# Kernel tuning notes

Hardware: AMD Instinct MI355X
Metric: run time of the kernel (lower is better)

Reference implementation:

```python
import jax
import jax.numpy as jnp
from jax import lax
import numpy as np

VOCAB = 50000
EMBED = 300
HIDDEN = 256
BATCH = 64
SEQ = 256
FORGET_BIAS = 1.0


def setup_inputs() -> dict:
    key = jax.random.key(0)
    k = jax.random.split(key, 6)
    x_in = jax.random.randint(k[0], (BATCH, SEQ), 0, VOCAB, dtype=jnp.int64)
    embedding = jax.random.normal(k[1], (VOCAB, EMBED), dtype=jnp.float32)
    W0 = jax.random.normal(k[2], (EMBED + HIDDEN, 4 * HIDDEN), dtype=jnp.float32) * 0.05
    b0 = jnp.zeros((4 * HIDDEN,), dtype=jnp.float32)
    W1 = jax.random.normal(k[3], (HIDDEN + HIDDEN, 4 * HIDDEN), dtype=jnp.float32) * 0.05
    b1 = jnp.zeros((4 * HIDDEN,), dtype=jnp.float32)
    return {"x_in": x_in, "embedding": embedding, "W0": W0, "b0": b0, "W1": W1, "b1": b1}


def _lstm_layer(xs, W, b):
    # xs: [B, T, D] -> hidden sequence [B, T, H] (BasicLSTMCell, gate order i,j,f,o)
    B = xs.shape[0]
    H = W.shape[1] // 4

    def step(carry, x_t):
        c, h = carry
        gates = jnp.dot(jnp.concatenate([x_t, h], axis=-1), W) + b  # [B, 4H]
        i, j, f, o = jnp.split(gates, 4, axis=-1)
        new_c = c * jax.nn.sigmoid(f + FORGET_BIAS) + jax.nn.sigmoid(i) * jnp.tanh(j)
        new_h = jnp.tanh(new_c) * jax.nn.sigmoid(o)
        return (new_c, new_h), new_h

    init = (jnp.zeros((B, H), xs.dtype), jnp.zeros((B, H), xs.dtype))
    _, hs = lax.scan(step, init, jnp.swapaxes(xs, 0, 1))  # hs: [T, B, H]
    return jnp.swapaxes(hs, 0, 1)


def reference(x_in, embedding, W0, b0, W1, b1):
    word_vecs = embedding[x_in]                 # [B, T, E] frozen embedding lookup
    h1 = _lstm_layer(word_vecs, W0, b0)         # layer 1
    h2 = _lstm_layer(h1, W1, b1)                # layer 2
    return h2[:, -1, :]                          # output at last timestep [B, H]
```

## Files before the change

kernel.cpp:

```cpp
#include <hip/hip_runtime.h>

#define EMBED   300
#define HIDDEN  256
#define SEQ     256
#define NG      1024
#define NL1     16
#define NL2     32
#define NBLK    112
#define CAP     (1 << 15)

typedef __attribute__((ext_vector_type(8))) short  short8;
typedef __attribute__((ext_vector_type(4))) float  f32x4;
typedef unsigned long long ull;

__device__ inline unsigned short f2bf(float f) {
    unsigned u = __builtin_bit_cast(unsigned, f);
    return (unsigned short)((u + 0x7FFFu + ((u >> 16) & 1u)) >> 16);
}
__device__ inline float bf2f(unsigned short h) {
    unsigned u = (unsigned)h << 16;
    return __builtin_bit_cast(float, u);
}
__device__ inline float sigm(float x)  { return 1.0f / (1.0f + __expf(-x)); }
__device__ inline float tanh_(float x) { return 2.0f / (1.0f + __expf(-2.0f * x)) - 1.0f; }
__device__ inline int swzb(int c, int base) { return base ^ (((c >> 1) & 3) << 4); }

__device__ inline unsigned ld32a(const unsigned* p) {
    return __hip_atomic_load(p, __ATOMIC_RELAXED, __HIP_MEMORY_SCOPE_AGENT);
}
__device__ inline void st32a(unsigned* p, unsigned v) {
    __hip_atomic_store(p, v, __ATOMIC_RELAXED, __HIP_MEMORY_SCOPE_AGENT);
}
__device__ inline ull ld64a(const ull* p) {
    return __hip_atomic_load(p, __ATOMIC_RELAXED, __HIP_MEMORY_SCOPE_AGENT);
}
__device__ inline void st64a(ull* p, ull v) {
    __hip_atomic_store(p, v, __ATOMIC_RELAXED, __HIP_MEMORY_SCOPE_AGENT);
}
__device__ inline float ldf32a(const float* p) {
    return __builtin_bit_cast(float, ld32a((const unsigned*)p));
}
__device__ inline void stf32a(float* p, float v) {
    st32a((unsigned*)p, __builtin_bit_cast(unsigned, v));
}
__device__ inline short8 ldh16a(const unsigned short* p) {
    ull t0 = ld64a((const ull*)p);
    ull t1 = ld64a((const ull*)p + 1);
    union { ull q[2]; short8 s; } u;
    u.q[0] = t0; u.q[1] = t1;
    return u.s;
}

#define MFMA(a, b, c) __builtin_amdgcn_mfma_f32_16x16x32_bf16((a), (b), (c), 0, 0, 0)

#define F1(i)    ((i) * 16)
#define F2(i)    ((16 + (i)) * 16)
#define FH(p, s) ((48 + (p) * 32 + (s)) * 16)

__global__ __launch_bounds__(256, 1) void lstm_v7(
    const int*   __restrict__ xin,
    const float* __restrict__ emb,
    const float* __restrict__ W0, const float* __restrict__ b0,
    const float* __restrict__ W1, const float* __restrict__ b1,
    unsigned*       __restrict__ flags,
    unsigned short* __restrict__ h1,
    unsigned short* __restrict__ h2,
    float*          __restrict__ ring1,
    float*          __restrict__ out)
{
    extern __shared__ char lds[];
    int* aliveP = (int*)(lds + 40960);
    const int tid = threadIdx.x, bid = blockIdx.x;
    const int w = tid >> 6, lane = tid & 63, l15 = lane & 15, q = lane >> 4;
    const int bbase = w * 16, arow = bbase + l15;
    bool alive = true;

    auto wpoll = [&](const unsigned* p0, unsigned t0,
                     const unsigned* p1, unsigned t1, float diag) -> bool {
        if (w == 0) {
            int n = 0;
            for (;;) {
                bool ok = ((p0 == nullptr) || (ld32a(p0) >= t0)) &&
                          ((p1 == nullptr) || (ld32a(p1) >= t1));
                if (__all(ok)) break;
                if (++n > CAP) { if (lane == 0) stf32a(out, diag); alive = false; break; }
            }
        }
        if (tid == 0) *aliveP = alive ? 1 : 0;
        __syncthreads();
        return *aliveP != 0;
    };
    auto drain_sync = [&]() {
        asm volatile("s_waitcnt vmcnt(0)" ::: "memory");
        __syncthreads();
    };

    if (bid < NL1) {
        const int u0 = bid * 16;
        { int r = tid >> 2, p = tid & 3;
          st64a((ull*)(h1 + 3 * 16384 + r * 256 + u0) + p, 0ULL); }
        short8 bfragR[8][4];
        #pragma unroll
        for (int s = 0; s < 8; ++s)
            #pragma unroll
            for (int nt = 0; nt < 4; ++nt)
                #pragma unroll
                for (int e2 = 0; e2 < 8; ++e2) {
                    int k = EMBED + s * 32 + q * 8 + e2;
                    bfragR[s][nt][e2] = (short)f2bf(W0[(long)k * NG + nt * 256 + u0 + l15]);
                }
        drain_sync();
        if (tid == 0) st32a(flags + F1(bid), 1u);

        {
            const unsigned* p0 = (lane < 32) ? flags + FH(0, lane) : nullptr;
            if (!wpoll(p0, 1u, nullptr, 0u, 52000.f)) return;
        }
        f32x4 gn[4];
        #pragma unroll
        for (int nt = 0; nt < 4; ++nt)
            #pragma unroll
            for (int rr = 0; rr < 4; ++rr)
                gn[nt][rr] = ldf32a(ring1 + (size_t)(bbase + q * 4 + rr) * NG + nt * 256 + u0 + l15);

        float c4[4] = {0.f, 0.f, 0.f, 0.f};
        for (int e = 0; e <= 255; ++e) {
            const unsigned* p0 = nullptr; unsigned t0 = 0;
            if (lane < 16) { p0 = flags + F1(lane); t0 = (unsigned)(e + 1); }
            else if (lane < 48 && e >= 4) { p0 = flags + F2(lane - 16); t0 = (unsigned)(e - 2); }
            const unsigned* p1 = (e <= 254 && lane < 32) ? flags + FH((e + 1) & 1, lane) : nullptr;
            if (!wpoll(p0, t0, p1, (unsigned)(e + 2), 51000.f + (float)e)) break;

            short8 a1[8];
            { const unsigned short* hb = h1 + ((e - 1) & 3) * 16384 + arow * 256;
              #pragma unroll
              for (int s = 0; s < 8; ++s) a1[s] = ldh16a(hb + s * 32 + q * 8); }

            f32x4 acc[4] = {gn[0], gn[1], gn[2], gn[3]};
            #pragma unroll
            for (int s = 0; s < 8; ++s)
                #pragma unroll
                for (int nt = 0; nt < 4; ++nt)
                    acc[nt] = MFMA(a1[s], bfragR[s][nt], acc[nt]);

            #pragma unroll
            for (int rr = 0; rr < 4; ++rr) {
                int b = bbase + q * 4 + rr;
                float iv = sigm(acc[0][rr]);
                float jv = tanh_(acc[1][rr]);
                float fv = sigm(acc[2][rr] + 1.0f);
                float ov = sigm(acc[3][rr]);
                float cn = c4[rr] * fv + iv * jv;
                c4[rr] = cn;
                *(unsigned short*)(lds + b * 32 + l15 * 2) = f2bf(tanh_(cn) * ov);
            }
            asm volatile("s_waitcnt lgkmcnt(0)" ::: "memory");
            {
                int r = bbase + (lane >> 2), p = lane & 3;
                ull v = *(ull*)(lds + r * 32 + p * 8);
                st64a((ull*)(h1 + (e & 3) * 16384 + r * 256 + u0) + p, v);
            }
            drain_sync();
            if (tid == 0) st32a(flags + F1(bid), (unsigned)(e + 2));

            if (e <= 254) {
                const float* g1 = ring1 + (size_t)((e + 1) & 3) * (64 * NG);
                #pragma unroll
                for (int nt = 0; nt < 4; ++nt)
                    #pragma unroll
                    for (int rr = 0; rr < 4; ++rr)
                        gn[nt][rr] = ldf32a(g1 + (size_t)(bbase + q * 4 + rr) * NG + nt * 256 + u0 + l15);
            }
        }

    } else if (bid < NL1 + NL2) {
        const int idx = bid - NL1, u0 = idx * 8;
        const int lo8 = l15 & 7;
        const bool gA = (l15 < 8);
        if (tid < 128) {
            int r = tid >> 1, p = tid & 1;
            st64a((ull*)(h2 + 16384 + r * 256 + u0) + p, 0ULL);
        }
        short8 bW1x[8][2], bW1r[8][2];
        float biasx[2];
        #pragma unroll
        for (int nt = 0; nt < 2; ++nt) {
            int col = (2 * nt + (l15 >> 3)) * 256 + u0 + lo8;
            biasx[nt] = b1[col];
            #pragma unroll
            for (int s = 0; s < 8; ++s)
                #pragma unroll
                for (int e2 = 0; e2 < 8; ++e2) {
                    int k = s * 32 + q * 8 + e2;
                    bW1x[s][nt][e2] = (short)f2bf(W1[(long)k * NG + col]);
                    bW1r[s][nt][e2] = (short)f2bf(W1[(long)(HIDDEN + k) * NG + col]);
                }
        }
        drain_sync();
        if (tid == 0) st32a(flags + F2(idx), 1u);

        float c4[4] = {0.f, 0.f, 0.f, 0.f};
        for (int t = 0; t <= 255; ++t) {
            const unsigned* p0 = nullptr; unsigned t0 = 0;
            if (lane < 16) { p0 = flags + F1(lane); t0 = (unsigned)(t + 2); }
            else if (lane < 48) { p0 = flags + F2(lane - 16); t0 = (unsigned)(t + 1); }
            if (!wpoll(p0, t0, nullptr, 0u, 54000.f + (float)t)) break;

            short8 a1[8], a2[8];
            const unsigned short* b1p = h1 + (t & 3) * 16384 + arow * 256;
            const unsigned short* b2p = h2 + ((t - 1) & 1) * 16384 + arow * 256;
            #pragma unroll
            for (int s = 0; s < 8; ++s) {
                a1[s] = ldh16a(b1p + s * 32 + q * 8);
                a2[s] = ldh16a(b2p + s * 32 + q * 8);
            }

            f32x4 acc[2] = { (f32x4){biasx[0], biasx[0], biasx[0], biasx[0]},
                             (f32x4){biasx[1], biasx[1], biasx[1], biasx[1]} };
            #pragma unroll
            for (int s = 0; s < 8; ++s)
                #pragma unroll
                for (int nt = 0; nt < 2; ++nt)
                    acc[nt] = MFMA(a1[s], bW1x[s][nt], acc[nt]);
            #pragma unroll
            for (int s = 0; s < 8; ++s)
                #pragma unroll
                for (int nt = 0; nt < 2; ++nt)
                    acc[nt] = MFMA(a2[s], bW1r[s][nt], acc[nt]);

            #pragma unroll
            for (int rr = 0; rr < 4; ++rr) {
                float x0 = acc[0][rr], x1 = acc[1][rr];
                float y0 = __shfl_xor(x0, 8), y1 = __shfl_xor(x1, 8);
                float iv = gA ? x0 : y0, jv = gA ? y0 : x0;
                float fv = gA ? x1 : y1, ov = gA ? y1 : x1;
                float cn = c4[rr] * sigm(fv + 1.f) + sigm(iv) * tanh_(jv);
                c4[rr] = cn;
                float hn = tanh_(cn) * sigm(ov);
                if (t == 255) {
                    if (gA) out[(bbase + q * 4 + rr) * 256 + u0 + lo8] = hn;
                } else {
                    if (gA) *(unsigned short*)(lds + w * 256 + (q * 4 + rr) * 16 + lo8 * 2) = f2bf(hn);
                }
            }
            if (t == 255) break;
            asm volatile("s_waitcnt lgkmcnt(0)" ::: "memory");
            if (q == 0) {
                ull v0 = *(ull*)(lds + w * 256 + l15 * 16);
                ull v1 = *(ull*)(lds + w * 256 + l15 * 16 + 8);
                ull* d = (ull*)(h2 + (t & 1) * 16384 + (bbase + l15) * 256 + u0);
                st64a(d, v0); st64a(d + 1, v1);
            }
            drain_sync();
            if (tid == 0) st32a(flags + F2(idx), (unsigned)(t + 2));
        }

    } else {
        const int hidx = bid - NL1 - NL2;
        const int par = hidx & 1, slice = hidx >> 1, hc0 = slice * 32;
        float biasH[2];
        #pragma unroll
        for (int gi = 0; gi < 2; ++gi) biasH[gi] = b0[hc0 + gi * 16 + l15];
        for (int i2 = tid; i2 < 20 * 32 * 32; i2 += 256) {
            int k = i2 >> 5, c = i2 & 31;
            int s = k >> 5, kk = k & 31;
            int row = (s >= 10) ? (k - 320) : k;
            float v = W0[(long)row * NG + hc0 + c];
            unsigned short hv = f2bf(v);
            if (s >= 10) hv = f2bf(v - bf2f(hv));
            *(unsigned short*)(lds + s * 2048 + swzb(c, c * 64 + kk * 2)) = hv;
        }
        __syncthreads();

        for (int t = par; t <= 255; t += 2) {
            int xid = xin[arow * SEQ + t];
            const float* erow = emb + (long)xid * EMBED;
            short8 ac[10];
            #pragma unroll
            for (int s = 0; s < 10; ++s) {
                int kb = s * 32 + q * 8;
                #pragma unroll
                for (int hh = 0; hh < 2; ++hh) {
                    int k4 = kb + hh * 4;
                    if (k4 < EMBED) {
                        f32x4 v = *(const f32x4*)(erow + k4);
                        #pragma unroll
                        for (int e2 = 0; e2 < 4; ++e2) ac[s][hh * 4 + e2] = (short)f2bf(v[e2]);
                    } else {
                        #pragma unroll
                        for (int e2 = 0; e2 < 4; ++e2) ac[s][hh * 4 + e2] = 0;
                    }
                }
            }
            f32x4 accg[2];
            #pragma unroll
            for (int gi = 0; gi < 2; ++gi)
                accg[gi] = (f32x4){biasH[gi], biasH[gi], biasH[gi], biasH[gi]};
            #pragma unroll
            for (int s = 0; s < 20; ++s) {
                short8 a = ac[(s < 10) ? s : s - 10];
                #pragma unroll
                for (int gi = 0; gi < 2; ++gi) {
                    int c = gi * 16 + l15;
                    short8 b = *(const short8*)(lds + s * 2048 + swzb(c, c * 64 + q * 16));
                    accg[gi] = MFMA(a, b, accg[gi]);
                }
            }
            if (t >= 4) {
                const unsigned* p0 = (lane < 16) ? flags + F1(lane) : nullptr;
                if (!wpoll(p0, (unsigned)(t - 2), nullptr, 0u, 55000.f + (float)t)) break;
            }
            float* dst = ring1 + (size_t)(t & 3) * (64 * NG);
            #pragma unroll
            for (int gi = 0; gi < 2; ++gi)
                #pragma unroll
                for (int rr = 0; rr < 4; ++rr)
                    stf32a(dst + (size_t)(bbase + q * 4 + rr) * NG + hc0 + gi * 16 + l15, accg[gi][rr]);
            drain_sync();
            if (tid == 0) st32a(flags + FH(par, slice), (unsigned)(t + 1));
        }
    }
}

__global__ void ws_too_small_sentinel(float* out, int n) {
    int i = blockIdx.x * 256 + threadIdx.x;
    if (i < n) out[i] = 31337.0f;
}

extern "C" void kernel_launch(void* const* d_in, const int* in_sizes, int n_in,
                              void* d_out, int out_size, void* d_ws, size_t ws_size,
                              hipStream_t stream)
{
    const int*   xin = (const int*)d_in[0];
    const float* emb = (const float*)d_in[1];
    const float* W0  = (const float*)d_in[2];
    const float* b0  = (const float*)d_in[3];
    const float* W1  = (const float*)d_in[4];
    const float* b1  = (const float*)d_in[5];
    float* out = (float*)d_out;

    const size_t OFF_FLAGS = 0;
    const size_t OFF_H1    = 8192;
    const size_t OFF_H2    = OFF_H1 + 131072;
    const size_t OFF_RING1 = OFF_H2 + 65536;
    const size_t NEED      = OFF_RING1 + (size_t)4 * 64 * NG * 4;

    if (ws_size < NEED) {
        ws_too_small_sentinel<<<(out_size + 255) / 256, 256, 0, stream>>>(out, out_size);
        return;
    }

    char* ws = (char*)d_ws;
    unsigned*       flags = (unsigned*)(ws + OFF_FLAGS);
    unsigned short* h1    = (unsigned short*)(ws + OFF_H1);
    unsigned short* h2    = (unsigned short*)(ws + OFF_H2);
    float*          ring1 = (float*)(ws + OFF_RING1);

    hipMemsetAsync(flags, 0, 8192, stream);
    lstm_v7<<<dim3(NBLK), dim3(256), 41088, stream>>>(
        xin, emb, W0, b0, W1, b1, flags, h1, h2, ring1, out);
}
```

Baseline: 1.616 ms.

## Halve layer-2 blocks, stage W1 input weights in LDS, pack flags densely

Layer 2 now runs on 16 blocks of 16 hidden units each instead of 32 blocks of 8. Each block computes all four gates locally, so the shuffle-based gate exchange goes away. The input-half of W1 no longer fits in registers at the larger width, so it is stored in swizzled LDS and read during the MFMA loop, while the recurrent half stays in registers. Flags are packed contiguously instead of one per 64 bytes, and the polling is reduced to a single flag per lane. The intent is fewer blocks to synchronise and less polling work on the recurrent critical path. The cost is more MFMA work per layer-2 block, extra LDS reads per step, and possible false sharing between the densely packed flags.

```diff
diff --git a/kernel.cpp b/kernel.cpp
--- a/kernel.cpp
+++ b/kernel.cpp
@@ -5,8 +5,8 @@
 #define SEQ     256
 #define NG      1024
 #define NL1     16
-#define NL2     32
-#define NBLK    112
+#define NL2     16
+#define NBLK    96
 #define CAP     (1 << 15)
 
 typedef __attribute__((ext_vector_type(8))) short  short8;
@@ -53,11 +53,11 @@
 
 #define MFMA(a, b, c) __builtin_amdgcn_mfma_f32_16x16x32_bf16((a), (b), (c), 0, 0, 0)
 
-#define F1(i)    ((i) * 16)
-#define F2(i)    ((16 + (i)) * 16)
-#define FH(p, s) ((48 + (p) * 32 + (s)) * 16)
-
-__global__ __launch_bounds__(256, 1) void lstm_v7(
+#define F1IX(i)    (i)
+#define F2IX(i)    (16 + (i))
+#define FHIX(p, s) (32 + (p) * 32 + (s))
+
+__global__ __launch_bounds__(256, 1) void lstm_v8(
     const int*   __restrict__ xin,
     const float* __restrict__ emb,
     const float* __restrict__ W0, const float* __restrict__ b0,
@@ -75,13 +75,11 @@
     const int bbase = w * 16, arow = bbase + l15;
     bool alive = true;
 
-    auto wpoll = [&](const unsigned* p0, unsigned t0,
-                     const unsigned* p1, unsigned t1, float diag) -> bool {
+    auto wpoll = [&](const unsigned* p0, unsigned t0, float diag) -> bool {
         if (w == 0) {
             int n = 0;
             for (;;) {
-                bool ok = ((p0 == nullptr) || (ld32a(p0) >= t0)) &&
-                          ((p1 == nullptr) || (ld32a(p1) >= t1));
+                bool ok = (p0 == nullptr) || (ld32a(p0) >= t0);
                 if (__all(ok)) break;
                 if (++n > CAP) { if (lane == 0) stf32a(out, diag); alive = false; break; }
             }
@@ -110,11 +108,11 @@
                     bfragR[s][nt][e2] = (short)f2bf(W0[(long)k * NG + nt * 256 + u0 + l15]);
                 }
         drain_sync();
-        if (tid == 0) st32a(flags + F1(bid), 1u);
+        if (tid == 0) st32a(flags + F1IX(bid), 1u);
 
         {
-            const unsigned* p0 = (lane < 32) ? flags + FH(0, lane) : nullptr;
-            if (!wpoll(p0, 1u, nullptr, 0u, 52000.f)) return;
+            const unsigned* p0 = (lane < 32) ? flags + FHIX(0, lane) : nullptr;
+            if (!wpoll(p0, 1u, 52000.f)) return;
         }
         f32x4 gn[4];
         #pragma unroll
@@ -126,10 +124,10 @@
         float c4[4] = {0.f, 0.f, 0.f, 0.f};
         for (int e = 0; e <= 255; ++e) {
             const unsigned* p0 = nullptr; unsigned t0 = 0;
-            if (lane < 16) { p0 = flags + F1(lane); t0 = (unsigned)(e + 1); }
-            else if (lane < 48 && e >= 4) { p0 = flags + F2(lane - 16); t0 = (unsigned)(e - 2); }
-            const unsigned* p1 = (e <= 254 && lane < 32) ? flags + FH((e + 1) & 1, lane) : nullptr;
-            if (!wpoll(p0, t0, p1, (unsigned)(e + 2), 51000.f + (float)e)) break;
+            if (lane < 16)      { p0 = flags + F1IX(lane); t0 = (unsigned)(e + 1); }
+            else if (lane < 32) { if (e >= 4) { p0 = flags + F2IX(lane - 16); t0 = (unsigned)(e - 2); } }
+            else                { if (e <= 254) { p0 = flags + FHIX((e + 1) & 1, lane - 32); t0 = (unsigned)(e + 2); } }
+            if (!wpoll(p0, t0, 51000.f + (float)e)) break;
 
             short8 a1[8];
             { const unsigned short* hb = h1 + ((e - 1) & 3) * 16384 + arow * 256;
@@ -161,7 +159,7 @@
                 st64a((ull*)(h1 + (e & 3) * 16384 + r * 256 + u0) + p, v);
             }
             drain_sync();
-            if (tid == 0) st32a(flags + F1(bid), (unsigned)(e + 2));
+            if (tid == 0) st32a(flags + F1IX(bid), (unsigned)(e + 2));
 
             if (e <= 254) {
                 const float* g1 = ring1 + (size_t)((e + 1) & 3) * (64 * NG);
@@ -174,37 +172,38 @@
         }
 
     } else if (bid < NL1 + NL2) {
-        const int idx = bid - NL1, u0 = idx * 8;
-        const int lo8 = l15 & 7;
-        const bool gA = (l15 < 8);
-        if (tid < 128) {
-            int r = tid >> 1, p = tid & 1;
-            st64a((ull*)(h2 + 16384 + r * 256 + u0) + p, 0ULL);
-        }
-        short8 bW1x[8][2], bW1r[8][2];
-        float biasx[2];
+        const int idx = bid - NL1, u0 = idx * 16, u = u0 + l15;
+        { int r = tid >> 2, p = tid & 3;
+          st64a((ull*)(h2 + 16384 + r * 256 + u0) + p, 0ULL); }
+        float biasx[4];
+        short8 bW1r[8][4];
         #pragma unroll
-        for (int nt = 0; nt < 2; ++nt) {
-            int col = (2 * nt + (l15 >> 3)) * 256 + u0 + lo8;
-            biasx[nt] = b1[col];
+        for (int nt = 0; nt < 4; ++nt) {
+            biasx[nt] = b1[nt * 256 + u0 + l15];
             #pragma unroll
             for (int s = 0; s < 8; ++s)
                 #pragma unroll
                 for (int e2 = 0; e2 < 8; ++e2) {
-                    int k = s * 32 + q * 8 + e2;
-                    bW1x[s][nt][e2] = (short)f2bf(W1[(long)k * NG + col]);
-                    bW1r[s][nt][e2] = (short)f2bf(W1[(long)(HIDDEN + k) * NG + col]);
-                }
+                    int k = HIDDEN + s * 32 + q * 8 + e2;
+                    bW1r[s][nt][e2] = (short)f2bf(W1[(long)k * NG + nt * 256 + u0 + l15]);
+                }
+        }
+        for (int i2 = tid; i2 < 8 * 64 * 32; i2 += 256) {
+            int k = i2 >> 6, c = i2 & 63;
+            int col = (c >> 4) * 256 + u0 + (c & 15);
+            int s = k >> 5, kk = k & 31;
+            *(unsigned short*)(lds + s * 4096 + swzb(c, c * 64 + kk * 2)) =
+                f2bf(W1[(long)k * NG + col]);
         }
         drain_sync();
-        if (tid == 0) st32a(flags + F2(idx), 1u);
+        if (tid == 0) st32a(flags + F2IX(idx), 1u);
 
         float c4[4] = {0.f, 0.f, 0.f, 0.f};
         for (int t = 0; t <= 255; ++t) {
             const unsigned* p0 = nullptr; unsigned t0 = 0;
-            if (lane < 16) { p0 = flags + F1(lane); t0 = (unsigned)(t + 2); }
-            else if (lane < 48) { p0 = flags + F2(lane - 16); t0 = (unsigned)(t + 1); }
-            if (!wpoll(p0, t0, nullptr, 0u, 54000.f + (float)t)) break;
+            if (lane < 16)      { p0 = flags + F1IX(lane); t0 = (unsigned)(t + 2); }
+            else if (lane < 32) { p0 = flags + F2IX(lane - 16); t0 = (unsigned)(t + 1); }
+            if (!wpoll(p0, t0, 54000.f + (float)t)) break;
 
             short8 a1[8], a2[8];
             const unsigned short* b1p = h1 + (t & 3) * 16384 + arow * 256;
@@ -215,44 +214,46 @@
                 a2[s] = ldh16a(b2p + s * 32 + q * 8);
             }
 
-            f32x4 acc[2] = { (f32x4){biasx[0], biasx[0], biasx[0], biasx[0]},
-                             (f32x4){biasx[1], biasx[1], biasx[1], biasx[1]} };
+            f32x4 acc[4];
+            #pragma unroll
+            for (int nt = 0; nt < 4; ++nt)
+                acc[nt] = (f32x4){biasx[nt], biasx[nt], biasx[nt], biasx[nt]};
             #pragma unroll
             for (int s = 0; s < 8; ++s)
                 #pragma unroll
-                for (int nt = 0; nt < 2; ++nt)
-                    acc[nt] = MFMA(a1[s], bW1x[s][nt], acc[nt]);
+                for (int nt = 0; nt < 4; ++nt) {
+                    int c = nt * 16 + l15;
+                    short8 bx = *(const short8*)(lds + s * 4096 + swzb(c, c * 64 + q * 16));
+                    acc[nt] = MFMA(a1[s], bx, acc[nt]);
+                }
             #pragma unroll
             for (int s = 0; s < 8; ++s)
                 #pragma unroll
-                for (int nt = 0; nt < 2; ++nt)
+                for (int nt = 0; nt < 4; ++nt)
                     acc[nt] = MFMA(a2[s], bW1r[s][nt], acc[nt]);
 
             #pragma unroll
             for (int rr = 0; rr < 4; ++rr) {
-                float x0 = acc[0][rr], x1 = acc[1][rr];
-                float y0 = __shfl_xor(x0, 8), y1 = __shfl_xor(x1, 8);
-                float iv = gA ? x0 : y0, jv = gA ? y0 : x0;
-                float fv = gA ? x1 : y1, ov = gA ? y1 : x1;
-                float cn = c4[rr] * sigm(fv + 1.f) + sigm(iv) * tanh_(jv);
+                int b = bbase + q * 4 + rr;
+                float iv = sigm(acc[0][rr]);
+                float jv = tanh_(acc[1][rr]);
+                float fv = sigm(acc[2][rr] + 1.0f);
+                float ov = sigm(acc[3][rr]);
+                float cn = c4[rr] * fv + iv * jv;
                 c4[rr] = cn;
-                float hn = tanh_(cn) * sigm(ov);
-                if (t == 255) {
-                    if (gA) out[(bbase + q * 4 + rr) * 256 + u0 + lo8] = hn;
-                } else {
-                    if (gA) *(unsigned short*)(lds + w * 256 + (q * 4 + rr) * 16 + lo8 * 2) = f2bf(hn);
-                }
+                float hn = tanh_(cn) * ov;
+                if (t == 255) out[b * HIDDEN + u] = hn;
+                else *(unsigned short*)(lds + 32768 + b * 32 + l15 * 2) = f2bf(hn);
             }
             if (t == 255) break;
             asm volatile("s_waitcnt lgkmcnt(0)" ::: "memory");
-            if (q == 0) {
-                ull v0 = *(ull*)(lds + w * 256 + l15 * 16);
-                ull v1 = *(ull*)(lds + w * 256 + l15 * 16 + 8);
-                ull* d = (ull*)(h2 + (t & 1) * 16384 + (bbase + l15) * 256 + u0);
-                st64a(d, v0); st64a(d + 1, v1);
+            {
+                int r = bbase + (lane >> 2), p = lane & 3;
+                ull v = *(ull*)(lds + 32768 + r * 32 + p * 8);
+                st64a((ull*)(h2 + (t & 1) * 16384 + r * 256 + u0) + p, v);
             }
             drain_sync();
-            if (tid == 0) st32a(flags + F2(idx), (unsigned)(t + 2));
+            if (tid == 0) st32a(flags + F2IX(idx), (unsigned)(t + 2));
         }
 
     } else {
@@ -307,8 +308,8 @@
                 }
             }
             if (t >= 4) {
-                const unsigned* p0 = (lane < 16) ? flags + F1(lane) : nullptr;
-                if (!wpoll(p0, (unsigned)(t - 2), nullptr, 0u, 55000.f + (float)t)) break;
+                const unsigned* p0 = (lane < 16) ? flags + F1IX(lane) : nullptr;
+                if (!wpoll(p0, (unsigned)(t - 2), 55000.f + (float)t)) break;
             }
             float* dst = ring1 + (size_t)(t & 3) * (64 * NG);
             #pragma unroll
@@ -317,7 +318,7 @@
                 for (int rr = 0; rr < 4; ++rr)
                     stf32a(dst + (size_t)(bbase + q * 4 + rr) * NG + hc0 + gi * 16 + l15, accg[gi][rr]);
             drain_sync();
-            if (tid == 0) st32a(flags + FH(par, slice), (unsigned)(t + 1));
+            if (tid == 0) st32a(flags + FHIX(par, slice), (unsigned)(t + 1));
         }
     }
 }
@@ -340,7 +341,7 @@
     float* out = (float*)d_out;
 
     const size_t OFF_FLAGS = 0;
-    const size_t OFF_H1    = 8192;
+    const size_t OFF_H1    = 4096;
     const size_t OFF_H2    = OFF_H1 + 131072;
     const size_t OFF_RING1 = OFF_H2 + 65536;
     const size_t NEED      = OFF_RING1 + (size_t)4 * 64 * NG * 4;
@@ -356,7 +357,7 @@
     unsigned short* h2    = (unsigned short*)(ws + OFF_H2);
     float*          ring1 = (float*)(ws + OFF_RING1);
 
-    hipMemsetAsync(flags, 0, 8192, stream);
-    lstm_v7<<<dim3(NBLK), dim3(256), 41088, stream>>>(
+    hipMemsetAsync(flags, 0, 4096, stream);
+    lstm_v8<<<dim3(NBLK), dim3(256), 41088, stream>>>(
         xin, emb, W0, b0, W1, b1, flags, h1, h2, ring1, out);
 }
```

Measured after the change: 1.766 ms. +9.3%, slower.
